# Kernel optimization log

Hardware: AMD Instinct MI355X
Metric: run time of the kernel (lower is better)

Reference implementation:

```python
import jax, jax.numpy as jnp
import numpy as np

B, T, F_, H = 128, 256, 36, 128
FREQ_INV = jnp.array([1.0 / 24.0, 1.0 / 168.0, 1.0 / 720.0], dtype=jnp.float32)
WRT = 0.1


def setup_inputs() -> dict:
    key = jax.random.key(0)
    ks = jax.random.split(key, 20)

    def unif(k, shape, s):
        return jax.random.uniform(k, shape, jnp.float32, -s, s)

    sH = 1.0 / np.sqrt(H)
    sF = 1.0 / np.sqrt(F_)
    s2F = 1.0 / np.sqrt(2 * F_)

    # data layout: [B, 24, T, F]; forward direction uses channels 0..11:
    # 0 originals, 1 masks (binary), 2 deltas (nonneg), 3/6/9 remainders,
    # 4/7/10 trends, 5/8/11 seasonals.
    data = jax.random.normal(ks[0], (B, 24, T, F_), dtype=jnp.float32)
    masks = (jax.random.uniform(ks[1], (B, T, F_)) > 0.2).astype(jnp.float32)
    deltas = jax.random.uniform(ks[2], (B, T, F_)) * 5.0
    data = data.at[:, 1, :, :].set(masks)
    data = data.at[:, 2, :, :].set(deltas)

    return {
        "data": data,
        "W_dh": unif(ks[3], (H, F_), sH),   # TemporalDecay(F->H)
        "b_dh": unif(ks[4], (H,), sH),
        "W_dx": unif(ks[5], (F_, F_), sF),  # TemporalDecay diag (F->F)
        "b_dx": unif(ks[6], (F_,), sF),
        "W_hist": unif(ks[7], (F_, H), sH),  # Linear(H, F)
        "b_hist": unif(ks[8], (F_,), sH),
        "W_feat": unif(ks[9], (F_, F_), sF),
        "b_feat": unif(ks[10], (F_,), sF),
        "W_wc": unif(ks[11], (F_, 2 * F_), s2F),  # Linear(2F, F)
        "b_wc": unif(ks[12], (F_,), s2F),
        "W_ih": unif(ks[13], (4 * H, 2 * F_), sH),  # LSTMCell
        "W_hh": unif(ks[14], (4 * H, H), sH),
        "b_ih": unif(ks[15], (4 * H,), sH),
        "b_hh": unif(ks[16], (4 * H,), sH),
        "W_comb": jax.random.normal(ks[17], (1, 3), dtype=jnp.float32),  # weight_sumone_linear(3,1)
    }


def reference(data, W_dh, b_dh, W_dx, b_dx, W_hist, b_hist, W_feat, b_feat,
              W_wc, b_wc, W_ih, W_hh, b_ih, b_hh, W_comb):
    Bn, _, Tn, Fd = data.shape
    Hh = W_hh.shape[1]

    masks = data[:, 1]   # [B,T,F]
    deltas = data[:, 2]
    r = jnp.stack([data[:, 3], data[:, 6], data[:, 9]], axis=1)    # [B,3,T,F]
    tr = jnp.stack([data[:, 4], data[:, 7], data[:, 10]], axis=1)
    se = jnp.stack([data[:, 5], data[:, 8], data[:, 11]], axis=1)

    # time-major for scan
    m_T = jnp.moveaxis(masks, 1, 0)    # [T,B,F]
    d_T = jnp.moveaxis(deltas, 1, 0)
    r_T = jnp.moveaxis(r, 2, 0)        # [T,B,3,F]
    tr_T = jnp.moveaxis(tr, 2, 0)
    se_T = jnp.moveaxis(se, 2, 0)

    wk = jax.nn.softmax(W_comb, axis=1)[0]          # [3], sums to 1
    Wf_masked = W_feat * (1.0 - jnp.eye(Fd, dtype=data.dtype))
    w_dx_diag = jnp.diagonal(W_dx)                   # diag TemporalDecay
    reg_term = WRT * jnp.sum(wk * FREQ_INV)          # added every timestep

    def comb(x):  # weight_sumone_linear over the 3-decomposition axis
        return jnp.einsum('bkf,k->bf', x, wk)

    def step(carry, xs):
        h, c, loss = carry
        m2, d2, rt, trt, st = xs
        m = jnp.broadcast_to(m2[:, None, :], rt.shape)  # [B,3,F]
        d = jnp.broadcast_to(d2[:, None, :], rt.shape)

        gamma_h = jnp.exp(-jax.nn.relu(jnp.einsum('bkf,hf->bkh', d, W_dh) + b_dh))
        gamma_x = jnp.exp(-jax.nn.relu(d * w_dx_diag + b_dx))
        h = h * gamma_h

        x_h = jnp.einsum('bkh,fh->bkf', h, W_hist) + b_hist
        denom = jnp.sum(comb(m)) + 1e-5
        loss = loss + jnp.sum(comb(jnp.abs(rt - x_h) * m)) / denom

        x_c = m * rt + (1.0 - m) * x_h
        z_h = jnp.einsum('bkf,gf->bkg', x_c, Wf_masked) + b_feat
        loss = loss + jnp.sum(comb(jnp.abs(rt - z_h) * m)) / denom

        alpha = jnp.einsum('bkf,gf->bkg', jnp.concatenate([gamma_x, m], axis=2), W_wc) + b_wc
        c_h = alpha * z_h + (1.0 - alpha) * x_h
        loss = loss + jnp.sum(comb(jnp.abs(rt - c_h) * m)) / denom
        loss = loss + reg_term

        c_c = m * rt + (1.0 - m) * c_h
        inp = jnp.concatenate([c_c, m], axis=2).reshape(-1, 2 * Fd)  # [B*3, 2F]
        hf = h.reshape(-1, Hh)
        cf = c.reshape(-1, Hh)
        # PyTorch LSTMCell: gates ordered i, f, g, o. (dropout is identity in eval)
        gates = inp @ W_ih.T + b_ih + hf @ W_hh.T + b_hh
        i, f, g, o = jnp.split(gates, 4, axis=1)
        cf = jax.nn.sigmoid(f) * cf + jax.nn.sigmoid(i) * jnp.tanh(g)
        hf = jax.nn.sigmoid(o) * jnp.tanh(cf)
        h = hf.reshape(-1, 3, Hh)
        c = cf.reshape(-1, 3, Hh)

        impute = comb(c_c + st + trt)  # [B,F]
        return (h, c, loss), impute

    h0 = jnp.zeros((Bn, 3, Hh), dtype=data.dtype)
    c0 = jnp.zeros((Bn, 3, Hh), dtype=data.dtype)
    (hT, cT, loss), imput_T = jax.lax.scan(
        step, (h0, c0, jnp.float32(0.0)), (m_T, d_T, r_T, tr_T, se_T))
    imputations = jnp.moveaxis(imput_T, 0, 1)  # [B,T,F]
    return loss, imputations
```

## Files before the change

kernel.cpp:

```cpp
#include <hip/hip_runtime.h>
#include <math.h>

#define Bn 128
#define Tn 256
#define Fn 36
#define Hn 128
#define G4 512
#define BTFn (Bn*Tn*Fn)
#define TF 9216

#define INVD_OFF 0
#define LOSS_OFF 102656
#define IMP_OFF  103040

#define OFF_WHIST  0
#define OFF_WF     2304
#define OFF_WWC    2952
#define OFF_WDHT   4248
#define OFF_IN     6552
#define OFF_DP     6732
#define OFF_MP     6752
#define OFF_GXP    6792
#define OFF_XCP    6812
#define OFF_CCP    6832
#define OFF_ALPHA  6852
#define OFF_HP     6888
#define OFF_GF     6952
#define OFF_INVD   7464
#define OFF_BH     7720
#define OFF_BF     7756
#define OFF_BWC    7792
#define OFF_BDH    7828
#define OFF_WDXD   7956
#define OFF_BDX    7992
#define SMEM_WORDS 8028

typedef _Float16 h2_t __attribute__((ext_vector_type(2)));

__device__ __forceinline__ unsigned int bcu(float x) { return __builtin_bit_cast(unsigned int, x); }
__device__ __forceinline__ unsigned int pkh(float a, float b) {
    return __builtin_bit_cast(unsigned int, __builtin_amdgcn_cvt_pkrtz(a, b));
}
__device__ __forceinline__ float dot2(unsigned int a, unsigned int b, float c) {
    return __builtin_amdgcn_fdot2(__builtin_bit_cast(h2_t, a), __builtin_bit_cast(h2_t, b), c, false);
}
__device__ __forceinline__ float sigmoid_f(float x) {
    return __builtin_amdgcn_rcpf(1.f + __expf(-x));
}
__device__ __forceinline__ float tanh_f(float x) {
    return fmaf(2.f, __builtin_amdgcn_rcpf(1.f + __expf(-2.f * x)), -1.f);
}

__global__ void prep_kernel(const float* __restrict__ data,
                            float* __restrict__ ws) {
    int t = blockIdx.x;
    int tid = threadIdx.x;
    __shared__ float red[256];
    float s = 0.f;
    for (int idx = tid; idx < Bn * Fn; idx += 256) {
        int b = idx / Fn, f = idx - b * Fn;
        s += data[((size_t)(b * 24 + 1) * Tn + t) * Fn + f];
    }
    red[tid] = s;
    __syncthreads();
    for (int off = 128; off > 0; off >>= 1) {
        if (tid < off) red[tid] += red[tid + off];
        __syncthreads();
    }
    if (tid == 0) ws[INVD_OFF + t] = 1.f / (red[0] + 1e-5f);
}

#define DOT18(acc, base, woff) do {                                    \
    const unsigned int* _p = &smem[(base)];                            \
    float _a = 0.f, _b = 0.f;                                          \
    float4 _v0 = *(const float4*)_p;                                   \
    _a = dot2(bcu(_v0.x), wi[(woff) + 0], _a);                         \
    _b = dot2(bcu(_v0.y), wi[(woff) + 1], _b);                         \
    _a = dot2(bcu(_v0.z), wi[(woff) + 2], _a);                         \
    _b = dot2(bcu(_v0.w), wi[(woff) + 3], _b);                         \
    float4 _v1 = *(const float4*)(_p + 4);                             \
    _a = dot2(bcu(_v1.x), wi[(woff) + 4], _a);                         \
    _b = dot2(bcu(_v1.y), wi[(woff) + 5], _b);                         \
    _a = dot2(bcu(_v1.z), wi[(woff) + 6], _a);                         \
    _b = dot2(bcu(_v1.w), wi[(woff) + 7], _b);                         \
    float4 _v2 = *(const float4*)(_p + 8);                             \
    _a = dot2(bcu(_v2.x), wi[(woff) + 8], _a);                         \
    _b = dot2(bcu(_v2.y), wi[(woff) + 9], _b);                         \
    _a = dot2(bcu(_v2.z), wi[(woff) + 10], _a);                        \
    _b = dot2(bcu(_v2.w), wi[(woff) + 11], _b);                        \
    float4 _v3 = *(const float4*)(_p + 12);                            \
    _a = dot2(bcu(_v3.x), wi[(woff) + 12], _a);                        \
    _b = dot2(bcu(_v3.y), wi[(woff) + 13], _b);                        \
    _a = dot2(bcu(_v3.z), wi[(woff) + 14], _a);                        \
    _b = dot2(bcu(_v3.w), wi[(woff) + 15], _b);                        \
    float2 _v4 = *(const float2*)(_p + 16);                            \
    _a = dot2(bcu(_v4.x), wi[(woff) + 16], _a);                        \
    _b = dot2(bcu(_v4.y), wi[(woff) + 17], _b);                        \
    acc += _a + _b;                                                    \
} while (0)

#define STAGE(v, P) do {                                                          \
    if (lw == 0) {                                                                \
        *(float2*)&smf[OFF_IN + 2 * lu] = (v);                                    \
        smem[OFF_MP + (P) * 20 + lu] = pkh((v).x, (v).y);                         \
    } else if (lw == 1) {                                                         \
        smem[OFF_DP + lu] = pkh((v).x, (v).y);                                    \
        float2 _wd = *(const float2*)&smf[OFF_WDXD + 2 * lu];                     \
        float2 _bd = *(const float2*)&smf[OFF_BDX + 2 * lu];                      \
        float _g0 = __expf(-fmaxf(fmaf((v).x, _wd.x, _bd.x), 0.f));               \
        float _g1 = __expf(-fmaxf(fmaf((v).y, _wd.y, _bd.y), 0.f));               \
        smem[OFF_GXP + lu] = pkh(_g0, _g1);                                       \
    } else {                                                                      \
        *(float2*)&smf[OFF_IN + lw * 36 + 2 * lu] = (v);                          \
    }                                                                             \
} while (0)

__global__ __launch_bounds__(512) void rits_main(
    const float* __restrict__ data,
    const float* __restrict__ W_dh, const float* __restrict__ b_dh,
    const float* __restrict__ W_dx, const float* __restrict__ b_dx,
    const float* __restrict__ W_hist, const float* __restrict__ b_hist,
    const float* __restrict__ W_feat, const float* __restrict__ b_feat,
    const float* __restrict__ W_wc, const float* __restrict__ b_wc,
    const float* __restrict__ W_ih, const float* __restrict__ W_hh,
    const float* __restrict__ b_ih, const float* __restrict__ b_hh,
    const float* __restrict__ W_comb,
    float* __restrict__ ws) {

    extern __shared__ unsigned int smem[];
    float* smf = (float*)smem;

    const int tid = threadIdx.x;
    const int chain = blockIdx.x;
    const int b = chain / 3, k = chain - 3 * b;

    for (int i = tid; i < 64 * Fn; i += 512) {
        int q = i / Fn, f = i - q * Fn;
        float2 wv = *(const float2*)&W_hist[f * Hn + 2 * q];
        smem[OFF_WHIST + i] = pkh(wv.x, wv.y);
    }
    for (int i = tid; i < 18 * Fn; i += 512) {
        int q = i / Fn, g = i - q * Fn;
        float2 wv = *(const float2*)&W_feat[g * Fn + 2 * q];
        float w0 = (2 * q     == g) ? 0.f : wv.x;
        float w1 = (2 * q + 1 == g) ? 0.f : wv.y;
        smem[OFF_WF + i] = pkh(w0, w1);
    }
    for (int i = tid; i < 36 * Fn; i += 512) {
        int q = i / Fn, g = i - q * Fn;
        int col = (q < 18) ? 2 * q : Fn + 2 * (q - 18);
        float2 wv = *(const float2*)&W_wc[g * 2 * Fn + col];
        smem[OFF_WWC + i] = pkh(wv.x, wv.y);
    }
    for (int i = tid; i < 18 * 128; i += 512) {
        int q = i >> 7, u = i & 127;
        float2 wv = *(const float2*)&W_dh[u * Fn + 2 * q];
        smem[OFF_WDHT + i] = pkh(wv.x, wv.y);
    }
    if (tid < Fn) {
        smf[OFF_BH + tid]   = b_hist[tid];
        smf[OFF_BF + tid]   = b_feat[tid];
        smf[OFF_BWC + tid]  = b_wc[tid];
        smf[OFF_WDXD + tid] = W_dx[tid * Fn + tid];
        smf[OFF_BDX + tid]  = b_dx[tid];
    }
    if (tid < Hn) smf[OFF_BDH + tid] = b_dh[tid];
    for (int i = tid; i < Tn; i += 512) smf[OFF_INVD + i] = ws[INVD_OFF + i];
    if (tid < 64) smem[OFF_HP + tid] = 0;

    unsigned int wh[64];
    #pragma unroll
    for (int q = 0; q < 64; ++q) {
        float2 wv = *(const float2*)&W_hh[tid * Hn + 2 * q];
        wh[q] = pkh(wv.x, wv.y);
    }
    unsigned int wi[36];
    #pragma unroll
    for (int q = 0; q < 36; ++q) {
        float2 wv = *(const float2*)&W_ih[tid * 2 * Fn + 2 * q];
        wi[q] = pkh(wv.x, wv.y);
    }
    const float bias_j = b_ih[tid] + b_hh[tid];

    const float* ldsrc = nullptr; int lw = 0, lu = 0;
    if (tid >= 64 && tid < 154) {
        int idx = tid - 64;
        lw = idx / 18; lu = idx - 18 * lw;
        int row = (lw == 0) ? 1 : (lw == 1) ? 2 : (3 + 3 * k + (lw - 2));
        ldsrc = data + (size_t)(b * 24 + row) * TF + 2 * lu;
    }
    float* impp = ws + IMP_OFF + (size_t)(k * Bn + b) * TF;

    float creg = 0.f, hreg = 0.f, loss_acc = 0.f, gm = 0.f;
    __syncthreads();

    float2 cur1 = {0,0}, cur2 = {0,0}, cur3 = {0,0};
    float2 nxt0 = {0,0}, nxt1 = {0,0}, nxt2 = {0,0}, nxt3 = {0,0};
    if (ldsrc) {
        float2 c0 = *(const float2*)(ldsrc);
        cur1 = *(const float2*)(ldsrc + Fn);
        cur2 = *(const float2*)(ldsrc + 2 * Fn);
        cur3 = *(const float2*)(ldsrc + 3 * Fn);
        STAGE(c0, 0);
    }
    __syncthreads();
    if (tid >= 128 && tid < 164) {
        int f = tid - 128;
        float a0 = smf[OFF_BWC + f], a1 = 0.f;
        #pragma unroll
        for (int q = 0; q < 18; ++q) {
            a0 = dot2(smem[OFF_GXP + q], smem[OFF_WWC + q * Fn + f], a0);
            a1 = dot2(smem[OFF_MP + q],  smem[OFF_WWC + (18 + q) * Fn + f], a1);
        }
        smf[OFF_ALPHA + f] = a0 + a1;
    }
    DOT18(gm, OFF_MP, 18);
    __syncthreads();

    for (int t8 = 0; t8 < Tn; t8 += 4) {
        float iv0 = 0.f, iv1 = 0.f, iv2 = 0.f, iv3 = 0.f;
        #pragma unroll
        for (int s = 0; s < 4; ++s) {
            const int t = t8 + s;
            const int par = s & 1, parn = par ^ 1;

            if (s == 0 && ldsrc) {
                nxt0 = *(const float2*)(ldsrc + (size_t)(t8 + 4) * Fn);
                nxt1 = *(const float2*)(ldsrc + (size_t)(t8 + 5) * Fn);
                nxt2 = *(const float2*)(ldsrc + (size_t)(t8 + 6) * Fn);
                nxt3 = *(const float2*)(ldsrc + (size_t)(t8 + 7) * Fn);
            }
            float gacc;
            {
                float g0 = 0.f, g1 = 0.f, g2 = 0.f, g3 = 0.f;
                #pragma unroll
                for (int q = 0; q < 64; q += 4) {
                    float4 hp = *(const float4*)&smem[OFF_HP + q];
                    g0 = dot2(bcu(hp.x), wh[q],     g0);
                    g1 = dot2(bcu(hp.y), wh[q + 1], g1);
                    g2 = dot2(bcu(hp.z), wh[q + 2], g2);
                    g3 = dot2(bcu(hp.w), wh[q + 3], g3);
                }
                gacc = (g0 + g1) + (g2 + g3);
            }
            if (tid < Fn) {
                float m  = smf[OFF_IN + tid];
                float rt = smf[OFF_IN + 72 + tid];
                float a0 = 0.f, a1 = 0.f, a2 = 0.f, a3 = 0.f;
                #pragma unroll
                for (int q = 0; q < 64; q += 4) {
                    unsigned int h0 = smem[OFF_HP + q];
                    unsigned int h1 = smem[OFF_HP + q + 1];
                    unsigned int h2 = smem[OFF_HP + q + 2];
                    unsigned int h3 = smem[OFF_HP + q + 3];
                    a0 = dot2(h0, smem[OFF_WHIST + q * Fn + tid], a0);
                    a1 = dot2(h1, smem[OFF_WHIST + (q + 1) * Fn + tid], a1);
                    a2 = dot2(h2, smem[OFF_WHIST + (q + 2) * Fn + tid], a2);
                    a3 = dot2(h3, smem[OFF_WHIST + (q + 3) * Fn + tid], a3);
                }
                float xh = (a0 + a1) + (a2 + a3) + smf[OFF_BH + tid];
                float xc = m * rt + (1.f - m) * xh;
                float xcn = __shfl_xor(xc, 1);
                if (!(tid & 1)) smem[OFF_XCP + (tid >> 1)] = pkh(xc, xcn);
                float z0 = 0.f, z1 = 0.f;
                #pragma unroll
                for (int q = 0; q < 18; q += 2) {
                    z0 = dot2(smem[OFF_XCP + q], smem[OFF_WF + q * Fn + tid], z0);
                    z1 = dot2(smem[OFF_XCP + q + 1], smem[OFF_WF + (q + 1) * Fn + tid], z1);
                }
                float zh = z0 + z1 + smf[OFF_BF + tid];
                float al = smf[OFF_ALPHA + tid];
                float chv = al * zh + (1.f - al) * xh;
                float cc = m * rt + (1.f - m) * chv;
                loss_acc = fmaf((fabsf(rt - xh) + fabsf(rt - zh) + fabsf(rt - chv)) * m,
                                smf[OFF_INVD + t], loss_acc);
                float ccn = __shfl_xor(cc, 1);
                if (!(tid & 1)) smem[OFF_CCP + (tid >> 1)] = pkh(cc, ccn);
                float iv = cc + smf[OFF_IN + 144 + tid] + smf[OFF_IN + 108 + tid];
                if (s == 0) iv0 = iv; else if (s == 1) iv1 = iv;
                else if (s == 2) iv2 = iv; else iv3 = iv;
            }
            __syncthreads();

            {
                float gA = gacc + gm + bias_j;
                DOT18(gA, OFF_CCP, 0);
                smf[OFF_GF + tid] = gA;
            }
            if (ldsrc) {
                if (s == 0) STAGE(cur1, parn);
                else if (s == 1) STAGE(cur2, parn);
                else if (s == 2) STAGE(cur3, parn);
                else STAGE(nxt0, parn);
            }
            __syncthreads();

            if (tid < Hn) {
                float ig = smf[OFF_GF + tid];
                float fg = smf[OFF_GF + 128 + tid];
                float gg = smf[OFF_GF + 256 + tid];
                float og = smf[OFF_GF + 384 + tid];
                creg = sigmoid_f(fg) * creg + sigmoid_f(ig) * tanh_f(gg);
                float hn_ = sigmoid_f(og) * tanh_f(creg);
                float g0 = smf[OFF_BDH + tid], g1 = 0.f;
                #pragma unroll
                for (int q = 0; q < 18; q += 2) {
                    g0 = dot2(smem[OFF_DP + q], smem[OFF_WDHT + q * 128 + tid], g0);
                    g1 = dot2(smem[OFF_DP + q + 1], smem[OFF_WDHT + (q + 1) * 128 + tid], g1);
                }
                hreg = hn_ * __expf(-fmaxf(g0 + g1, 0.f));
                float hn2 = __shfl_xor(hreg, 1);
                if (!(tid & 1)) smem[OFF_HP + (tid >> 1)] = pkh(hreg, hn2);
            } else if (tid < 164) {
                int f = tid - 128;
                float a0 = smf[OFF_BWC + f], a1 = 0.f;
                #pragma unroll
                for (int q = 0; q < 18; ++q) {
                    a0 = dot2(smem[OFF_GXP + q], smem[OFF_WWC + q * Fn + f], a0);
                    a1 = dot2(smem[OFF_MP + parn * 20 + q], smem[OFF_WWC + (18 + q) * Fn + f], a1);
                }
                smf[OFF_ALPHA + f] = a0 + a1;
            }
            gm = 0.f;
            DOT18(gm, OFF_MP + parn * 20, 18);
            __syncthreads();

            if (s == 3 && tid < Fn) {
                impp[(size_t)t8 * Fn + tid]       = iv0;
                impp[(size_t)(t8 + 1) * Fn + tid] = iv1;
                impp[(size_t)(t8 + 2) * Fn + tid] = iv2;
                impp[(size_t)(t8 + 3) * Fn + tid] = iv3;
            }
        }
        if (ldsrc) { cur1 = nxt1; cur2 = nxt2; cur3 = nxt3; }
    }

    if (tid < Fn) smf[OFF_GF + tid] = loss_acc;
    __syncthreads();
    if (tid == 0) {
        float s = 0.f;
        for (int i = 0; i < Fn; ++i) s += smf[OFF_GF + i];
        float w0 = W_comb[0], w1 = W_comb[1], w2 = W_comb[2];
        float mx = fmaxf(w0, fmaxf(w1, w2));
        float e0 = expf(w0 - mx), e1 = expf(w1 - mx), e2 = expf(w2 - mx);
        float wkk = ((k == 0) ? e0 : (k == 1) ? e1 : e2) / (e0 + e1 + e2);
        ws[LOSS_OFF + chain] = s * wkk;
    }
}

__global__ void impute_reduce(const float* __restrict__ ws,
                              const float* __restrict__ W_comb,
                              float* __restrict__ out) {
    int idx = blockIdx.x * 256 + threadIdx.x;
    float w0 = W_comb[0], w1 = W_comb[1], w2 = W_comb[2];
    float mx = fmaxf(w0, fmaxf(w1, w2));
    float e0 = expf(w0 - mx), e1 = expf(w1 - mx), e2 = expf(w2 - mx);
    float inv = 1.f / (e0 + e1 + e2);
    const float* imp = ws + IMP_OFF;
    out[1 + idx] = (e0 * imp[idx] + e1 * imp[BTFn + idx] + e2 * imp[2 * BTFn + idx]) * inv;
}

__global__ void loss_final(const float* __restrict__ ws,
                           const float* __restrict__ W_comb,
                           float* __restrict__ out) {
    int tid = threadIdx.x;
    __shared__ float red[512];
    const float* lp = ws + LOSS_OFF;
    red[tid] = (tid < 384) ? lp[tid] : 0.f;
    __syncthreads();
    for (int off = 256; off > 0; off >>= 1) {
        if (tid < off) red[tid] += red[tid + off];
        __syncthreads();
    }
    if (tid == 0) {
        float w0 = W_comb[0], w1 = W_comb[1], w2 = W_comb[2];
        float mx = fmaxf(w0, fmaxf(w1, w2));
        float e0 = expf(w0 - mx), e1 = expf(w1 - mx), e2 = expf(w2 - mx);
        float inv = 1.f / (e0 + e1 + e2);
        float wk0 = e0 * inv, wk1 = e1 * inv, wk2 = e2 * inv;
        float reg = 0.1f * (wk0 * (1.f / 24.f) + wk1 * (1.f / 168.f) + wk2 * (1.f / 720.f));
        out[0] = red[0] + (float)Tn * reg;
    }
}

extern "C" void kernel_launch(void* const* d_in, const int* in_sizes, int n_in,
                              void* d_out, int out_size, void* d_ws, size_t ws_size,
                              hipStream_t stream) {
    const float* data   = (const float*)d_in[0];
    const float* W_dh   = (const float*)d_in[1];
    const float* b_dh   = (const float*)d_in[2];
    const float* W_dx   = (const float*)d_in[3];
    const float* b_dx   = (const float*)d_in[4];
    const float* W_hist = (const float*)d_in[5];
    const float* b_hist = (const float*)d_in[6];
    const float* W_feat = (const float*)d_in[7];
    const float* b_feat = (const float*)d_in[8];
    const float* W_wc   = (const float*)d_in[9];
    const float* b_wc   = (const float*)d_in[10];
    const float* W_ih   = (const float*)d_in[11];
    const float* W_hh   = (const float*)d_in[12];
    const float* b_ih   = (const float*)d_in[13];
    const float* b_hh   = (const float*)d_in[14];
    const float* W_comb = (const float*)d_in[15];
    float* ws = (float*)d_ws;
    float* out = (float*)d_out;

    hipLaunchKernelGGL(prep_kernel, dim3(Tn), dim3(256), 0, stream, data, ws);
    hipLaunchKernelGGL(rits_main, dim3(Bn * 3), dim3(512), SMEM_WORDS * 4, stream,
                       data, W_dh, b_dh, W_dx, b_dx, W_hist, b_hist,
                       W_feat, b_feat, W_wc, b_wc, W_ih, W_hh, b_ih, b_hh, W_comb, ws);
    hipLaunchKernelGGL(impute_reduce, dim3(BTFn / 256), dim3(256), 0, stream, ws, W_comb, out);
    hipLaunchKernelGGL(loss_final, dim3(1), dim3(512), 0, stream, ws, W_comb, out);
}
```

Before: 1.016 ms.

## Remap LSTM gate rows per wavefront and exchange gates via shuffles, removing a barrier

Reassigns each thread's LSTM gate row so that the i, f, g and o gates of 16 hidden units sit in one 64-lane wavefront. The gates are then gathered with cross-lane shuffles instead of being written to shared memory, which removes the gate staging buffer and one __syncthreads per timestep. Staged inputs, deltas and decay factors are double-buffered by parity so the next step's staging can overlap the current step's reads. In exchange, the cell update now runs on 16 lanes in every wavefront instead of in the first two wavefronts, and the alpha computation is moved to other threads.

```diff
diff --git a/kernel.cpp b/kernel.cpp
--- a/kernel.cpp
+++ b/kernel.cpp
@@ -5,7 +5,6 @@
 #define Tn 256
 #define Fn 36
 #define Hn 128
-#define G4 512
 #define BTFn (Bn*Tn*Fn)
 #define TF 9216
 
@@ -18,22 +17,21 @@
 #define OFF_WWC    2952
 #define OFF_WDHT   4248
 #define OFF_IN     6552
-#define OFF_DP     6732
-#define OFF_MP     6752
-#define OFF_GXP    6792
-#define OFF_XCP    6812
-#define OFF_CCP    6832
-#define OFF_ALPHA  6852
-#define OFF_HP     6888
-#define OFF_GF     6952
-#define OFF_INVD   7464
-#define OFF_BH     7720
-#define OFF_BF     7756
-#define OFF_BWC    7792
-#define OFF_BDH    7828
-#define OFF_WDXD   7956
-#define OFF_BDX    7992
-#define SMEM_WORDS 8028
+#define OFF_DP     6912
+#define OFF_MP     6952
+#define OFF_GXP    6992
+#define OFF_XCP    7032
+#define OFF_CCP    7052
+#define OFF_ALPHA  7072
+#define OFF_HP     7108
+#define OFF_INVD   7172
+#define OFF_BH     7428
+#define OFF_BF     7464
+#define OFF_BWC    7500
+#define OFF_BDH    7536
+#define OFF_WDXD   7664
+#define OFF_BDX    7700
+#define SMEM_WORDS 7736
 
 typedef _Float16 h2_t __attribute__((ext_vector_type(2)));
 
@@ -101,17 +99,17 @@
 
 #define STAGE(v, P) do {                                                          \
     if (lw == 0) {                                                                \
-        *(float2*)&smf[OFF_IN + 2 * lu] = (v);                                    \
+        *(float2*)&smf[OFF_IN + (P) * 180 + 2 * lu] = (v);                        \
         smem[OFF_MP + (P) * 20 + lu] = pkh((v).x, (v).y);                         \
     } else if (lw == 1) {                                                         \
-        smem[OFF_DP + lu] = pkh((v).x, (v).y);                                    \
+        smem[OFF_DP + (P) * 20 + lu] = pkh((v).x, (v).y);                         \
         float2 _wd = *(const float2*)&smf[OFF_WDXD + 2 * lu];                     \
         float2 _bd = *(const float2*)&smf[OFF_BDX + 2 * lu];                      \
         float _g0 = __expf(-fmaxf(fmaf((v).x, _wd.x, _bd.x), 0.f));               \
         float _g1 = __expf(-fmaxf(fmaf((v).y, _wd.y, _bd.y), 0.f));               \
-        smem[OFF_GXP + lu] = pkh(_g0, _g1);                                       \
+        smem[OFF_GXP + (P) * 20 + lu] = pkh(_g0, _g1);                            \
     } else {                                                                      \
-        *(float2*)&smf[OFF_IN + lw * 36 + 2 * lu] = (v);                          \
+        *(float2*)&smf[OFF_IN + (P) * 180 + lw * 36 + 2 * lu] = (v);              \
     }                                                                             \
 } while (0)
 
@@ -131,31 +129,35 @@
     float* smf = (float*)smem;
 
     const int tid = threadIdx.x;
+    const int lane = tid & 63;
+    const int wv = tid >> 6;
+    const int unit = wv * 16 + (lane & 15);
+    const int row_j = unit + 128 * (lane >> 4);
     const int chain = blockIdx.x;
     const int b = chain / 3, k = chain - 3 * b;
 
     for (int i = tid; i < 64 * Fn; i += 512) {
         int q = i / Fn, f = i - q * Fn;
-        float2 wv = *(const float2*)&W_hist[f * Hn + 2 * q];
-        smem[OFF_WHIST + i] = pkh(wv.x, wv.y);
+        float2 wvv = *(const float2*)&W_hist[f * Hn + 2 * q];
+        smem[OFF_WHIST + i] = pkh(wvv.x, wvv.y);
     }
     for (int i = tid; i < 18 * Fn; i += 512) {
         int q = i / Fn, g = i - q * Fn;
-        float2 wv = *(const float2*)&W_feat[g * Fn + 2 * q];
-        float w0 = (2 * q     == g) ? 0.f : wv.x;
-        float w1 = (2 * q + 1 == g) ? 0.f : wv.y;
+        float2 wvv = *(const float2*)&W_feat[g * Fn + 2 * q];
+        float w0 = (2 * q     == g) ? 0.f : wvv.x;
+        float w1 = (2 * q + 1 == g) ? 0.f : wvv.y;
         smem[OFF_WF + i] = pkh(w0, w1);
     }
     for (int i = tid; i < 36 * Fn; i += 512) {
         int q = i / Fn, g = i - q * Fn;
         int col = (q < 18) ? 2 * q : Fn + 2 * (q - 18);
-        float2 wv = *(const float2*)&W_wc[g * 2 * Fn + col];
-        smem[OFF_WWC + i] = pkh(wv.x, wv.y);
+        float2 wvv = *(const float2*)&W_wc[g * 2 * Fn + col];
+        smem[OFF_WWC + i] = pkh(wvv.x, wvv.y);
     }
     for (int i = tid; i < 18 * 128; i += 512) {
         int q = i >> 7, u = i & 127;
-        float2 wv = *(const float2*)&W_dh[u * Fn + 2 * q];
-        smem[OFF_WDHT + i] = pkh(wv.x, wv.y);
+        float2 wvv = *(const float2*)&W_dh[u * Fn + 2 * q];
+        smem[OFF_WDHT + i] = pkh(wvv.x, wvv.y);
     }
     if (tid < Fn) {
         smf[OFF_BH + tid]   = b_hist[tid];
@@ -171,16 +173,16 @@
     unsigned int wh[64];
     #pragma unroll
     for (int q = 0; q < 64; ++q) {
-        float2 wv = *(const float2*)&W_hh[tid * Hn + 2 * q];
-        wh[q] = pkh(wv.x, wv.y);
+        float2 wvv = *(const float2*)&W_hh[row_j * Hn + 2 * q];
+        wh[q] = pkh(wvv.x, wvv.y);
     }
     unsigned int wi[36];
     #pragma unroll
     for (int q = 0; q < 36; ++q) {
-        float2 wv = *(const float2*)&W_ih[tid * 2 * Fn + 2 * q];
-        wi[q] = pkh(wv.x, wv.y);
-    }
-    const float bias_j = b_ih[tid] + b_hh[tid];
+        float2 wvv = *(const float2*)&W_ih[row_j * 2 * Fn + 2 * q];
+        wi[q] = pkh(wvv.x, wvv.y);
+    }
+    const float bias_j = b_ih[row_j] + b_hh[row_j];
 
     const float* ldsrc = nullptr; int lw = 0, lu = 0;
     if (tid >= 64 && tid < 154) {
@@ -191,7 +193,7 @@
     }
     float* impp = ws + IMP_OFF + (size_t)(k * Bn + b) * TF;
 
-    float creg = 0.f, hreg = 0.f, loss_acc = 0.f, gm = 0.f;
+    float creg = 0.f, loss_acc = 0.f, gm = 0.f;
     __syncthreads();
 
     float2 cur1 = {0,0}, cur2 = {0,0}, cur3 = {0,0};
@@ -204,8 +206,8 @@
         STAGE(c0, 0);
     }
     __syncthreads();
-    if (tid >= 128 && tid < 164) {
-        int f = tid - 128;
+    if (tid >= 144 && tid < 180) {
+        int f = tid - 144;
         float a0 = smf[OFF_BWC + f], a1 = 0.f;
         #pragma unroll
         for (int q = 0; q < 18; ++q) {
@@ -244,8 +246,9 @@
                 gacc = (g0 + g1) + (g2 + g3);
             }
             if (tid < Fn) {
-                float m  = smf[OFF_IN + tid];
-                float rt = smf[OFF_IN + 72 + tid];
+                const int inb = OFF_IN + par * 180;
+                float m  = smf[inb + tid];
+                float rt = smf[inb + 72 + tid];
                 float a0 = 0.f, a1 = 0.f, a2 = 0.f, a3 = 0.f;
                 #pragma unroll
                 for (int q = 0; q < 64; q += 4) {
@@ -276,16 +279,9 @@
                                 smf[OFF_INVD + t], loss_acc);
                 float ccn = __shfl_xor(cc, 1);
                 if (!(tid & 1)) smem[OFF_CCP + (tid >> 1)] = pkh(cc, ccn);
-                float iv = cc + smf[OFF_IN + 144 + tid] + smf[OFF_IN + 108 + tid];
+                float iv = cc + smf[inb + 144 + tid] + smf[inb + 108 + tid];
                 if (s == 0) iv0 = iv; else if (s == 1) iv1 = iv;
                 else if (s == 2) iv2 = iv; else iv3 = iv;
-            }
-            __syncthreads();
-
-            {
-                float gA = gacc + gm + bias_j;
-                DOT18(gA, OFF_CCP, 0);
-                smf[OFF_GF + tid] = gA;
             }
             if (ldsrc) {
                 if (s == 0) STAGE(cur1, parn);
@@ -295,31 +291,35 @@
             }
             __syncthreads();
 
-            if (tid < Hn) {
-                float ig = smf[OFF_GF + tid];
-                float fg = smf[OFF_GF + 128 + tid];
-                float gg = smf[OFF_GF + 256 + tid];
-                float og = smf[OFF_GF + 384 + tid];
-                creg = sigmoid_f(fg) * creg + sigmoid_f(ig) * tanh_f(gg);
-                float hn_ = sigmoid_f(og) * tanh_f(creg);
-                float g0 = smf[OFF_BDH + tid], g1 = 0.f;
-                #pragma unroll
-                for (int q = 0; q < 18; q += 2) {
-                    g0 = dot2(smem[OFF_DP + q], smem[OFF_WDHT + q * 128 + tid], g0);
-                    g1 = dot2(smem[OFF_DP + q + 1], smem[OFF_WDHT + (q + 1) * 128 + tid], g1);
+            {
+                float gate = gacc + gm + bias_j;
+                DOT18(gate, OFF_CCP, 0);
+                const int base = lane & 15;
+                float fg = __shfl(gate, base + 16, 64);
+                float gg = __shfl(gate, base + 32, 64);
+                float og = __shfl(gate, base + 48, 64);
+                if (lane < 16) {
+                    creg = sigmoid_f(fg) * creg + sigmoid_f(gate) * tanh_f(gg);
+                    float hn_ = sigmoid_f(og) * tanh_f(creg);
+                    float g0 = smf[OFF_BDH + unit], g1 = 0.f;
+                    #pragma unroll
+                    for (int q = 0; q < 18; q += 2) {
+                        g0 = dot2(smem[OFF_DP + parn * 20 + q], smem[OFF_WDHT + q * 128 + unit], g0);
+                        g1 = dot2(smem[OFF_DP + parn * 20 + q + 1], smem[OFF_WDHT + (q + 1) * 128 + unit], g1);
+                    }
+                    float hreg = hn_ * __expf(-fmaxf(g0 + g1, 0.f));
+                    float hn2 = __shfl_xor(hreg, 1);
+                    if (!(lane & 1)) smem[OFF_HP + (unit >> 1)] = pkh(hreg, hn2);
+                } else if (tid >= 144 && tid < 180) {
+                    int f = tid - 144;
+                    float a0 = smf[OFF_BWC + f], a1 = 0.f;
+                    #pragma unroll
+                    for (int q = 0; q < 18; ++q) {
+                        a0 = dot2(smem[OFF_GXP + parn * 20 + q], smem[OFF_WWC + q * Fn + f], a0);
+                        a1 = dot2(smem[OFF_MP + parn * 20 + q], smem[OFF_WWC + (18 + q) * Fn + f], a1);
+                    }
+                    smf[OFF_ALPHA + f] = a0 + a1;
                 }
-                hreg = hn_ * __expf(-fmaxf(g0 + g1, 0.f));
-                float hn2 = __shfl_xor(hreg, 1);
-                if (!(tid & 1)) smem[OFF_HP + (tid >> 1)] = pkh(hreg, hn2);
-            } else if (tid < 164) {
-                int f = tid - 128;
-                float a0 = smf[OFF_BWC + f], a1 = 0.f;
-                #pragma unroll
-                for (int q = 0; q < 18; ++q) {
-                    a0 = dot2(smem[OFF_GXP + q], smem[OFF_WWC + q * Fn + f], a0);
-                    a1 = dot2(smem[OFF_MP + parn * 20 + q], smem[OFF_WWC + (18 + q) * Fn + f], a1);
-                }
-                smf[OFF_ALPHA + f] = a0 + a1;
             }
             gm = 0.f;
             DOT18(gm, OFF_MP + parn * 20, 18);
@@ -335,11 +335,12 @@
         if (ldsrc) { cur1 = nxt1; cur2 = nxt2; cur3 = nxt3; }
     }
 
-    if (tid < Fn) smf[OFF_GF + tid] = loss_acc;
+    __syncthreads();
+    if (tid < Fn) smf[OFF_IN + tid] = loss_acc;
     __syncthreads();
     if (tid == 0) {
         float s = 0.f;
-        for (int i = 0; i < Fn; ++i) s += smf[OFF_GF + i];
+        for (int i = 0; i < Fn; ++i) s += smf[OFF_IN + i];
         float w0 = W_comb[0], w1 = W_comb[1], w2 = W_comb[2];
         float mx = fmaxf(w0, fmaxf(w1, w2));
         float e0 = expf(w0 - mx), e1 = expf(w1 - mx), e2 = expf(w2 - mx);
```

Result: slower. 1.584 ms (+56.0%).
